# Performance work log

Hardware: AMD Instinct MI355X
Metric: run time of the kernel (lower is better)

## Reference

```python
import jax, jax.numpy as jnp
import numpy as np

D = 128          # feature / hidden dim
K = 3            # SortPooling k (hard-coded in Topkpool)
NUM_CLASS = 10
EPS = 1e-5       # BatchNorm eps


def setup_inputs() -> dict:
    key = jax.random.key(0)
    ks = jax.random.split(key, 24)
    G, NPG = 512, 200
    N = G * NPG
    E = 1638400
    inp = {
        "x": jax.random.normal(ks[0], (N, D), jnp.float32),
        "src": jax.random.randint(ks[1], (E,), 0, N),
        "dst": jax.random.randint(ks[2], (E,), 0, N),
        "num_graphs": G,
        "nodes_per_graph": NPG,
    }
    s = 1.0 / np.sqrt(D)
    for i in (1, 2, 3):
        inp[f"W{i}"] = jax.random.uniform(ks[2 + i], (D, D), jnp.float32, -s, s)
        inp[f"b{i}"] = jnp.zeros((D,), jnp.float32)
        inp[f"g{i}"] = jnp.ones((D,), jnp.float32)   # BN gamma
        inp[f"bt{i}"] = jnp.zeros((D,), jnp.float32)  # BN beta
    sp = 1.0 / np.sqrt(K * D)
    for i in range(4):
        inp[f"P{i}w"] = jax.random.uniform(ks[10 + i], (K * D, NUM_CLASS), jnp.float32, -sp, sp)
        inp[f"P{i}b"] = jnp.zeros((NUM_CLASS,), jnp.float32)
    return inp


def _graph_conv(h, src, dst, W, b, n):
    # DGL GraphConv, norm='both': D_in^{-1/2} A (D_out^{-1/2} h) W + b
    one = jnp.ones((src.shape[0],), h.dtype)
    deg_out = jnp.zeros((n,), h.dtype).at[src].add(one)
    deg_in = jnp.zeros((n,), h.dtype).at[dst].add(one)
    h = h * jax.lax.rsqrt(jnp.maximum(deg_out, 1.0))[:, None]
    agg = jax.ops.segment_sum(h[src], dst, num_segments=n)  # [N, D] scatter-add
    agg = agg * jax.lax.rsqrt(jnp.maximum(deg_in, 1.0))[:, None]
    return agg @ W + b


def _bn_relu(h, g, bt):
    mu = h.mean(axis=0)
    var = jnp.mean((h - mu) ** 2, axis=0)  # biased var, torch BN training mode
    return jax.nn.relu((h - mu) * jax.lax.rsqrt(var + EPS) * g + bt)


def _sort_pool(h, G, npg):
    # DGL SortPooling: sort each node's feature vector ascending, then pick
    # top-K nodes per graph by last (max) channel, concatenate features.
    d = h.shape[-1]
    hs = jnp.sort(h, axis=-1).reshape(G, npg, d)
    idx = jax.lax.top_k(hs[:, :, -1], K)[1]                       # [G, K]
    return jnp.take_along_axis(hs, idx[:, :, None], axis=1).reshape(G, K * d)


def reference(x, W1, b1, g1, bt1, W2, b2, g2, bt2, W3, b3, g3, bt3,
              P0w, P0b, P1w, P1b, P2w, P2b, P3w, P3b,
              src, dst, num_graphs, nodes_per_graph):
    n = x.shape[0]
    reps = [x]
    h = x
    for W, b, g, bt in ((W1, b1, g1, bt1), (W2, b2, g2, bt2), (W3, b3, g3, bt3)):
        h = _bn_relu(_graph_conv(h, src, dst, W, b, n), g, bt)
        reps.append(h)
    score = jnp.zeros((num_graphs, NUM_CLASS), x.dtype)
    for h_i, Pw, Pb in zip(reps, (P0w, P1w, P2w, P3w), (P0b, P1b, P2b, P3b)):
        score = score + _sort_pool(h_i, num_graphs, nodes_per_graph) @ Pw + Pb
    return score
```

## Files before the change

### kernel.cpp

```cpp
#include <hip/hip_runtime.h>
#include <hip/hip_bf16.h>

#define D 128
#define KTOP 3
#define NCLS 10
#define EPS 1e-5f
#define GBM 128
#define BCAP 64


__global__ __launch_bounds__(256) void prologue_kernel(
        const int* __restrict__ src,
        int* __restrict__ deg_out, int E,
        const float* __restrict__ x, float* __restrict__ nodemax, int N,
        float* __restrict__ score, const float* __restrict__ pb0,
        const float* __restrict__ pb1, const float* __restrict__ pb2,
        const float* __restrict__ pb3, int G) {
    int b = blockIdx.x;
    int nbDeg = (E + 255) >> 8;
    if (b < nbDeg) {
        int e = b * 256 + threadIdx.x;
        if (e < E) atomicAdd(&deg_out[src[e]], 1);
        return;
    }
    b -= nbDeg;
    int nbR = N >> 3;
    if (b < nbR) {
        int node = b * 8 + (threadIdx.x >> 5);
        int l = threadIdx.x & 31;
        float4 v = *reinterpret_cast<const float4*>(x + (size_t)node * D + 4 * l);
        float m = fmaxf(fmaxf(v.x, v.y), fmaxf(v.z, v.w));
#pragma unroll
        for (int d = 16; d > 0; d >>= 1) m = fmaxf(m, __shfl_xor(m, d, 64));
        if (l == 0) nodemax[node] = m;
        return;
    }
    for (int i = threadIdx.x; i < G * NCLS; i += 256) {
        int c = i % NCLS;
        score[i] = pb0[c] + pb1[c] + pb2[c] + pb3[c];
    }
}

__global__ void rs_out_kernel(const int* __restrict__ deg_out,
                              float* __restrict__ rs_out, int N) {
    int i = blockIdx.x * blockDim.x + threadIdx.x;
    if (i >= N) return;
    int a = deg_out[i]; if (a < 1) a = 1;
    rs_out[i] = rsqrtf((float)a);
}

__global__ void csr_scatter(const int* __restrict__ src, const int* __restrict__ dst,
                            const float* __restrict__ rs_out,
                            int* __restrict__ cursor, int2* __restrict__ csrw, int E) {
    int e = blockIdx.x * blockDim.x + threadIdx.x;
    if (e >= E) return;
    int d = dst[e], s = src[e];
    int slot = atomicAdd(&cursor[d], 1);
    if (slot >= BCAP) return;
    int2 p; p.x = s; p.y = __float_as_int(rs_out[s]);
    csrw[(size_t)d * BCAP + slot] = p;
}

__global__ void pad_kernel(const int* __restrict__ cursor, int2* __restrict__ csrw, int N) {
    int d = blockIdx.x * blockDim.x + threadIdx.x;
    if (d >= N) return;
    int c = cursor[d]; if (c > BCAP) c = BCAP;
    int end = (c + 7) & ~7;
    int2 z; z.x = 0; z.y = 0;
    for (int i = c; i < end; ++i) csrw[(size_t)d * BCAP + i] = z;
}


__global__ __launch_bounds__(256) void aggregate_head(
        const float* __restrict__ hin, const int* __restrict__ cursor,
        const int2* __restrict__ csrw, float* __restrict__ hout, int nHalf,
        const float* __restrict__ nodemax, const float* __restrict__ Pw,
        float* __restrict__ score, int NPG) {
    __shared__ float ov[256];
    __shared__ float sv[256];
    __shared__ int   si[256];
    __shared__ int   sel[KTOP];
    __shared__ float sbuf[KTOP][D];
    __shared__ float red[4][NCLS];
    int b = blockIdx.x;
    int t = threadIdx.x;
    int nAgg = 2 * nHalf;
    if (b < nAgg) {
        int pass = (b >= nHalf) ? 1 : 0;
        int nb = pass ? b - nHalf : b;
        int node = nb * 16 + (t >> 4);
        int l = t & 15;
        int colOff = (pass << 6) + 4 * l;
        int deg = cursor[node];
        int end = (deg + 7) & ~7;
        const int2* bkt = csrw + (size_t)node * BCAP;
        const float* base = hin + colOff;
        float4 a0 = {0.f, 0.f, 0.f, 0.f}, a1 = a0;
        for (int e = 0; e < end; e += 8) {
            const int4* ce = reinterpret_cast<const int4*>(bkt + e);
            int4 p0 = ce[0], p1 = ce[1], p2 = ce[2], p3 = ce[3];
            float4 v0 = *reinterpret_cast<const float4*>(base + (size_t)p0.x * D);
            float4 v1 = *reinterpret_cast<const float4*>(base + (size_t)p0.z * D);
            float4 v2 = *reinterpret_cast<const float4*>(base + (size_t)p1.x * D);
            float4 v3 = *reinterpret_cast<const float4*>(base + (size_t)p1.z * D);
            float4 v4 = *reinterpret_cast<const float4*>(base + (size_t)p2.x * D);
            float4 v5 = *reinterpret_cast<const float4*>(base + (size_t)p2.z * D);
            float4 v6 = *reinterpret_cast<const float4*>(base + (size_t)p3.x * D);
            float4 v7 = *reinterpret_cast<const float4*>(base + (size_t)p3.z * D);
            float w0 = __int_as_float(p0.y), w1 = __int_as_float(p0.w);
            float w2 = __int_as_float(p1.y), w3 = __int_as_float(p1.w);
            float w4 = __int_as_float(p2.y), w5 = __int_as_float(p2.w);
            float w6 = __int_as_float(p3.y), w7 = __int_as_float(p3.w);
            a0.x += w0*v0.x; a0.y += w0*v0.y; a0.z += w0*v0.z; a0.w += w0*v0.w;
            a1.x += w1*v1.x; a1.y += w1*v1.y; a1.z += w1*v1.z; a1.w += w1*v1.w;
            a0.x += w2*v2.x; a0.y += w2*v2.y; a0.z += w2*v2.z; a0.w += w2*v2.w;
            a1.x += w3*v3.x; a1.y += w3*v3.y; a1.z += w3*v3.z; a1.w += w3*v3.w;
            a0.x += w4*v4.x; a0.y += w4*v4.y; a0.z += w4*v4.z; a0.w += w4*v4.w;
            a1.x += w5*v5.x; a1.y += w5*v5.y; a1.z += w5*v5.z; a1.w += w5*v5.w;
            a0.x += w6*v6.x; a0.y += w6*v6.y; a0.z += w6*v6.z; a0.w += w6*v6.w;
            a1.x += w7*v7.x; a1.y += w7*v7.y; a1.z += w7*v7.z; a1.w += w7*v7.w;
        }
        float ri = rsqrtf((float)(deg < 1 ? 1 : deg));
        float4 r;
        r.x = (a0.x + a1.x) * ri;
        r.y = (a0.y + a1.y) * ri;
        r.z = (a0.z + a1.z) * ri;
        r.w = (a0.w + a1.w) * ri;
        *reinterpret_cast<float4*>(hout + (size_t)node * D + colOff) = r;
        return;
    }

    int gr = b - nAgg;
    ov[t] = (t < NPG) ? nodemax[(size_t)gr * NPG + t] : -3.4e38f;
    __syncthreads();
    for (int ks = 0; ks < KTOP; ++ks) {
        sv[t] = ov[t]; si[t] = t;
        __syncthreads();
        for (int s = 128; s > 0; s >>= 1) {
            if (t < s) {
                float a = sv[t], c = sv[t + s];
                int ia = si[t], ib = si[t + s];
                if (c > a || (c == a && ib < ia)) { sv[t] = c; si[t] = ib; }
            }
            __syncthreads();
        }
        if (t == 0) { sel[ks] = si[0]; ov[si[0]] = -3.4e38f; }
        __syncthreads();
    }
    int u = t >> 7, tl = t & 127;
    sbuf[u][tl] = hin[((size_t)gr * NPG + sel[u]) * D + tl];
    if (t < 128) sbuf[2][t] = hin[((size_t)gr * NPG + sel[2]) * D + t];
    __syncthreads();
    for (int size = 2; size <= D; size <<= 1) {
        for (int stride = size >> 1; stride > 0; stride >>= 1) {
            int ixj = tl ^ stride;
            if (ixj > tl) {
                float a = sbuf[u][tl], c = sbuf[u][ixj];
                bool up = ((tl & size) == 0);
                if ((a > c) == up) { sbuf[u][tl] = c; sbuf[u][ixj] = a; }
            }
            if (t < 128) {
                int ix2 = t ^ stride;
                if (ix2 > t) {
                    float a = sbuf[2][t], c = sbuf[2][ix2];
                    bool up = ((t & size) == 0);
                    if ((a > c) == up) { sbuf[2][t] = c; sbuf[2][ix2] = a; }
                }
            }
            __syncthreads();
        }
    }
    float part[NCLS];
    float v0 = sbuf[u][tl];
    const float* pw0 = Pw + (size_t)(u * D + tl) * NCLS;
#pragma unroll
    for (int c = 0; c < NCLS; ++c) part[c] = v0 * pw0[c];
    if (t < 128) {
        float v2 = sbuf[2][t];
        const float* pw2 = Pw + (size_t)(2 * D + t) * NCLS;
#pragma unroll
        for (int c = 0; c < NCLS; ++c) part[c] += v2 * pw2[c];
    }
    int lane = t & 63, wid = t >> 6;
#pragma unroll
    for (int c = 0; c < NCLS; ++c) {
        float xx = part[c];
#pragma unroll
        for (int o = 32; o > 0; o >>= 1) xx += __shfl_down(xx, o, 64);
        if (lane == 0) red[wid][c] = xx;
    }
    __syncthreads();
    if (t < NCLS)
        atomicAdd(&score[gr * NCLS + t],
                  red[0][t] + red[1][t] + red[2][t] + red[3][t]);
}


__device__ __forceinline__ void gemm_chunk(const float* __restrict__ ain, size_t rowBase,
        int kc, int c0, const float (*Wl)[D], float (&acc)[4][8]) {
#pragma unroll 2
    for (int k4 = 0; k4 < 16; ++k4) {
        const float* ap = ain + rowBase * D + kc + 4 * k4;
        float4 a0 = *reinterpret_cast<const float4*>(ap);
        float4 a1 = *reinterpret_cast<const float4*>(ap + D);
        float4 a2 = *reinterpret_cast<const float4*>(ap + 2 * D);
        float4 a3 = *reinterpret_cast<const float4*>(ap + 3 * D);
#pragma unroll
        for (int j = 0; j < 4; ++j) {
            int kk = 4 * k4 + j;
            float4 w0 = *reinterpret_cast<const float4*>(&Wl[kk][c0]);
            float4 w1 = *reinterpret_cast<const float4*>(&Wl[kk][c0 + 4]);
            float av[4];
            av[0] = (j==0)?a0.x:(j==1)?a0.y:(j==2)?a0.z:a0.w;
            av[1] = (j==0)?a1.x:(j==1)?a1.y:(j==2)?a1.z:a1.w;
            av[2] = (j==0)?a2.x:(j==1)?a2.y:(j==2)?a2.z:a2.w;
            av[3] = (j==0)?a3.x:(j==1)?a3.y:(j==2)?a3.z:a3.w;
            float wv[8] = {w0.x, w0.y, w0.z, w0.w, w1.x, w1.y, w1.z, w1.w};
#pragma unroll
            for (int i = 0; i < 4; ++i)
#pragma unroll
                for (int jj = 0; jj < 8; ++jj) acc[i][jj] += av[i] * wv[jj];
        }
    }
}

__global__ __launch_bounds__(512) void gemm_bn(const float* __restrict__ ain,
        const float* __restrict__ W, const float* __restrict__ bias,
        float* __restrict__ hout, float* __restrict__ bnsums, int N) {
    __shared__ __align__(16) float Wl[64][D];
    int t = threadIdx.x;
    int cg = t & 15;
    int rs = t >> 4;
    int c0 = cg * 8;
    size_t rowBase = (size_t)blockIdx.x * GBM + 4 * rs;

    float acc[4][8];
#pragma unroll
    for (int i = 0; i < 4; ++i)
#pragma unroll
        for (int j = 0; j < 8; ++j) acc[i][j] = 0.f;

    const float4* Wv = reinterpret_cast<const float4*>(W);
    float4* Wd = reinterpret_cast<float4*>(&Wl[0][0]);
    float4 wpre[4];
#pragma unroll
    for (int i = 0; i < 4; ++i) wpre[i] = Wv[t + 512 * i];
#pragma unroll
    for (int i = 0; i < 4; ++i) Wd[t + 512 * i] = wpre[i];
#pragma unroll
    for (int i = 0; i < 4; ++i) wpre[i] = Wv[2048 + t + 512 * i];
    __syncthreads();
    gemm_chunk(ain, rowBase, 0, c0, Wl, acc);
    __syncthreads();
#pragma unroll
    for (int i = 0; i < 4; ++i) Wd[t + 512 * i] = wpre[i];
    __syncthreads();
    gemm_chunk(ain, rowBase, 64, c0, Wl, acc);

    float4 b0 = *reinterpret_cast<const float4*>(&bias[c0]);
    float4 b1 = *reinterpret_cast<const float4*>(&bias[c0 + 4]);
    float bv[8] = {b0.x, b0.y, b0.z, b0.w, b1.x, b1.y, b1.z, b1.w};
    float cs[8], cq[8];
#pragma unroll
    for (int j = 0; j < 8; ++j) { cs[j] = 0.f; cq[j] = 0.f; }
#pragma unroll
    for (int i = 0; i < 4; ++i) {
#pragma unroll
        for (int j = 0; j < 8; ++j) {
            float v = acc[i][j] + bv[j];
            acc[i][j] = v;
            cs[j] += v;
            cq[j] += v * v;
        }
    }
#pragma unroll
    for (int i = 0; i < 4; ++i) {
        size_t row = rowBase + i;
        float4 o0, o1;
        o0.x = acc[i][0]; o0.y = acc[i][1]; o0.z = acc[i][2]; o0.w = acc[i][3];
        o1.x = acc[i][4]; o1.y = acc[i][5]; o1.z = acc[i][6]; o1.w = acc[i][7];
        *reinterpret_cast<float4*>(&hout[row * D + c0])     = o0;
        *reinterpret_cast<float4*>(&hout[row * D + c0 + 4]) = o1;
    }
#pragma unroll
    for (int j = 0; j < 8; ++j) {
        cs[j] += __shfl_xor(cs[j], 16, 64); cq[j] += __shfl_xor(cq[j], 16, 64);
        cs[j] += __shfl_xor(cs[j], 32, 64); cq[j] += __shfl_xor(cq[j], 32, 64);
    }
    __syncthreads();
    float* red = &Wl[0][0];
    int wid = t >> 6, lane = t & 63;
    if (lane < 16) {
#pragma unroll
        for (int j = 0; j < 8; ++j) {
            red[wid * 256 + lane * 16 + j]     = cs[j];
            red[wid * 256 + lane * 16 + 8 + j] = cq[j];
        }
    }
    __syncthreads();
    if (t < 256) {
        float s = 0.f;
#pragma unroll
        for (int w = 0; w < 8; ++w) s += red[w * 256 + t];
        int cgi = t >> 4, r = t & 15;
        int ch = cgi * 8 + (r & 7);
        atomicAdd(&bnsums[(r < 8 ? 0 : D) + ch], s);
    }
}


__global__ __launch_bounds__(256) void bn_apply_relu_max(float* __restrict__ h,
        const float* __restrict__ bnsums, const float* __restrict__ g,
        const float* __restrict__ bt, float* __restrict__ nodemax, int N, float invN) {
    __shared__ float sc[D], sh[D];
    int t = threadIdx.x;
    if (t < D) {
        float mu  = bnsums[t] * invN;
        float var = bnsums[D + t] * invN - mu * mu;
        float inv = rsqrtf(var + EPS);
        float s = g[t] * inv;
        sc[t] = s;
        sh[t] = bt[t] - mu * s;
    }
    __syncthreads();
    int node = (blockIdx.x * 256 + t) >> 5;
    int l = t & 31;
    if (node >= N) return;
    float4 v = *reinterpret_cast<const float4*>(h + (size_t)node * D + 4 * l);
    float4 a = *reinterpret_cast<const float4*>(&sc[4 * l]);
    float4 b = *reinterpret_cast<const float4*>(&sh[4 * l]);
    v.x = fmaxf(fmaf(v.x, a.x, b.x), 0.f);
    v.y = fmaxf(fmaf(v.y, a.y, b.y), 0.f);
    v.z = fmaxf(fmaf(v.z, a.z, b.z), 0.f);
    v.w = fmaxf(fmaf(v.w, a.w, b.w), 0.f);
    *reinterpret_cast<float4*>(h + (size_t)node * D + 4 * l) = v;
    float m = fmaxf(fmaxf(v.x, v.y), fmaxf(v.z, v.w));
#pragma unroll
    for (int d = 16; d > 0; d >>= 1) m = fmaxf(m, __shfl_xor(m, d, 64));
    if (l == 0) nodemax[node] = m;
}


extern "C" void kernel_launch(void* const* d_in, const int* in_sizes, int n_in,
                              void* d_out, int out_size, void* d_ws, size_t ws_size,
                              hipStream_t stream) {
    const float* x   = (const float*)d_in[0];
    const int*   src = (const int*)d_in[1];
    const int*   dst = (const int*)d_in[2];
    const float* W[3]  = {(const float*)d_in[5],  (const float*)d_in[9],  (const float*)d_in[13]};
    const float* bb[3] = {(const float*)d_in[6],  (const float*)d_in[10], (const float*)d_in[14]};
    const float* gg[3] = {(const float*)d_in[7],  (const float*)d_in[11], (const float*)d_in[15]};
    const float* bt[3] = {(const float*)d_in[8],  (const float*)d_in[12], (const float*)d_in[16]};
    const float* Pw[4] = {(const float*)d_in[17], (const float*)d_in[19], (const float*)d_in[21], (const float*)d_in[23]};
    const float* Pb[4] = {(const float*)d_in[18], (const float*)d_in[20], (const float*)d_in[22], (const float*)d_in[24]};

    int N = in_sizes[0] / D;
    int E = in_sizes[1];
    int G = out_size / NCLS;
    int NPG = N / G;
    float* score = (float*)d_out;

    size_t NF = (size_t)N * D;
    float* fws     = (float*)d_ws;
    float* H       = fws;
    float* T       = H + NF;
    float* rs_out  = T + NF;
    float* nodemax = rs_out + N;
    float* bnsums  = nodemax + N;
    int* deg_out = (int*)(bnsums + 6 * D);
    int* cursor  = deg_out + N;
    int2* csrw   = (int2*)(cursor + N);

    int nbDeg = (E + 255) >> 8;
    int nbR = N >> 3;
    float invN = 1.0f / (float)N;

    hipMemsetAsync(deg_out, 0, sizeof(int) * (size_t)2 * N, stream);
    hipMemsetAsync(bnsums, 0, sizeof(float) * 6 * D, stream);

    prologue_kernel<<<nbDeg + nbR + 1, 256, 0, stream>>>(
        src, deg_out, E, x, nodemax, N,
        score, Pb[0], Pb[1], Pb[2], Pb[3], G);
    rs_out_kernel<<<(N + 255) / 256, 256, 0, stream>>>(deg_out, rs_out, N);
    csr_scatter<<<(E + 255) / 256, 256, 0, stream>>>(src, dst, rs_out, cursor, csrw, E);
    pad_kernel<<<(N + 255) / 256, 256, 0, stream>>>(cursor, csrw, N);

    int nHalf = N / 16;
    const float* hin = x;
    for (int l = 0; l < 3; ++l) {
        float* bns = bnsums + l * 2 * D;
        aggregate_head<<<2 * nHalf + G, 256, 0, stream>>>(
            hin, cursor, csrw, T, nHalf, nodemax, Pw[l], score, NPG);
        gemm_bn<<<N / GBM, 512, 0, stream>>>(T, W[l], bb[l], H, bns, N);
        bn_apply_relu_max<<<N / 8, 256, 0, stream>>>(H, bns, gg[l], bt[l], nodemax, N, invN);
        hin = H;
    }
    aggregate_head<<<G, 256, 0, stream>>>(
        H, cursor, csrw, T, 0, nodemax, Pw[3], score, NPG);
}
```

Before: 830.7 us.

## Fuse CSR build into prologue, defer weight fill, widen aggregation to full rows

The dst-bucketed CSR scatter now runs inside the prologue kernel alongside the out-degree count, and only source indices are stored. A new wfill_pad kernel fills the rsqrt(deg_out) weights and zero-pads each bucket, which removes the rs_out array and two separate launches. Aggregation now uses 32 lanes per node covering all 128 columns instead of two half-column passes, so each bucket's index list is read once rather than twice. The capped loop bound also avoids overrunning a bucket when the degree exceeds BCAP.

```diff
diff --git a/kernel.cpp b/kernel.cpp
--- a/kernel.cpp
+++ b/kernel.cpp
@@ -10,8 +10,9 @@
 
 
 __global__ __launch_bounds__(256) void prologue_kernel(
-        const int* __restrict__ src,
-        int* __restrict__ deg_out, int E,
+        const int* __restrict__ src, const int* __restrict__ dst,
+        int* __restrict__ deg_out, int* __restrict__ cursor,
+        int2* __restrict__ csrw, int E,
         const float* __restrict__ x, float* __restrict__ nodemax, int N,
         float* __restrict__ score, const float* __restrict__ pb0,
         const float* __restrict__ pb1, const float* __restrict__ pb2,
@@ -24,6 +25,17 @@
         return;
     }
     b -= nbDeg;
+    if (b < nbDeg) {
+        int e = b * 256 + threadIdx.x;
+        if (e < E) {
+            int d = dst[e];
+            int slot = atomicAdd(&cursor[d], 1);
+            if (slot < BCAP)
+                reinterpret_cast<int*>(csrw)[((size_t)d * BCAP + slot) * 2] = src[e];
+        }
+        return;
+    }
+    b -= nbDeg;
     int nbR = N >> 3;
     if (b < nbR) {
         int node = b * 8 + (threadIdx.x >> 5);
@@ -41,39 +53,29 @@
     }
 }
 
-__global__ void rs_out_kernel(const int* __restrict__ deg_out,
-                              float* __restrict__ rs_out, int N) {
-    int i = blockIdx.x * blockDim.x + threadIdx.x;
-    if (i >= N) return;
-    int a = deg_out[i]; if (a < 1) a = 1;
-    rs_out[i] = rsqrtf((float)a);
-}
-
-__global__ void csr_scatter(const int* __restrict__ src, const int* __restrict__ dst,
-                            const float* __restrict__ rs_out,
-                            int* __restrict__ cursor, int2* __restrict__ csrw, int E) {
-    int e = blockIdx.x * blockDim.x + threadIdx.x;
-    if (e >= E) return;
-    int d = dst[e], s = src[e];
-    int slot = atomicAdd(&cursor[d], 1);
-    if (slot >= BCAP) return;
-    int2 p; p.x = s; p.y = __float_as_int(rs_out[s]);
-    csrw[(size_t)d * BCAP + slot] = p;
-}
-
-__global__ void pad_kernel(const int* __restrict__ cursor, int2* __restrict__ csrw, int N) {
-    int d = blockIdx.x * blockDim.x + threadIdx.x;
-    if (d >= N) return;
-    int c = cursor[d]; if (c > BCAP) c = BCAP;
-    int end = (c + 7) & ~7;
-    int2 z; z.x = 0; z.y = 0;
-    for (int i = c; i < end; ++i) csrw[(size_t)d * BCAP + i] = z;
+
+__global__ __launch_bounds__(256) void wfill_pad(const int* __restrict__ cursor,
+        const int* __restrict__ deg_out, int2* __restrict__ csrw, int N) {
+    int node = blockIdx.x * 4 + (threadIdx.x >> 6);
+    int slot = threadIdx.x & 63;
+    if (node >= N) return;
+    int c = cursor[node]; if (c > BCAP) c = BCAP;
+    int cpad = (c + 7) & ~7;
+    int2* ent = csrw + (size_t)node * BCAP + slot;
+    if (slot < c) {
+        int s = ent->x;
+        int dg = deg_out[s]; if (dg < 1) dg = 1;
+        ent->y = __float_as_int(rsqrtf((float)dg));
+    } else if (slot < cpad) {
+        int2 z; z.x = 0; z.y = 0;
+        *ent = z;
+    }
 }
 
 
 __global__ __launch_bounds__(256) void aggregate_head(
         const float* __restrict__ hin, const int* __restrict__ cursor,
-        const int2* __restrict__ csrw, float* __restrict__ hout, int nHalf,
+        const int2* __restrict__ csrw, float* __restrict__ hout, int nAgg,
         const float* __restrict__ nodemax, const float* __restrict__ Pw,
         float* __restrict__ score, int NPG) {
     __shared__ float ov[256];
@@ -84,17 +86,13 @@
     __shared__ float red[4][NCLS];
     int b = blockIdx.x;
     int t = threadIdx.x;
-    int nAgg = 2 * nHalf;
     if (b < nAgg) {
-        int pass = (b >= nHalf) ? 1 : 0;
-        int nb = pass ? b - nHalf : b;
-        int node = nb * 16 + (t >> 4);
-        int l = t & 15;
-        int colOff = (pass << 6) + 4 * l;
+        int node = b * 8 + (t >> 5);
+        int l = t & 31;
         int deg = cursor[node];
-        int end = (deg + 7) & ~7;
+        int end = (deg + 7) & ~7; if (end > BCAP) end = BCAP;
         const int2* bkt = csrw + (size_t)node * BCAP;
-        const float* base = hin + colOff;
+        const float* base = hin + 4 * l;
         float4 a0 = {0.f, 0.f, 0.f, 0.f}, a1 = a0;
         for (int e = 0; e < end; e += 8) {
             const int4* ce = reinterpret_cast<const int4*>(bkt + e);
@@ -126,7 +124,7 @@
         r.y = (a0.y + a1.y) * ri;
         r.z = (a0.z + a1.z) * ri;
         r.w = (a0.w + a1.w) * ri;
-        *reinterpret_cast<float4*>(hout + (size_t)node * D + colOff) = r;
+        *reinterpret_cast<float4*>(hout + (size_t)node * D + 4 * l) = r;
         return;
     }
 
@@ -364,8 +362,7 @@
     float* fws     = (float*)d_ws;
     float* H       = fws;
     float* T       = H + NF;
-    float* rs_out  = T + NF;
-    float* nodemax = rs_out + N;
+    float* nodemax = T + NF;
     float* bnsums  = nodemax + N;
     int* deg_out = (int*)(bnsums + 6 * D);
     int* cursor  = deg_out + N;
@@ -378,19 +375,17 @@
     hipMemsetAsync(deg_out, 0, sizeof(int) * (size_t)2 * N, stream);
     hipMemsetAsync(bnsums, 0, sizeof(float) * 6 * D, stream);
 
-    prologue_kernel<<<nbDeg + nbR + 1, 256, 0, stream>>>(
-        src, deg_out, E, x, nodemax, N,
+    prologue_kernel<<<2 * nbDeg + nbR + 1, 256, 0, stream>>>(
+        src, dst, deg_out, cursor, csrw, E, x, nodemax, N,
         score, Pb[0], Pb[1], Pb[2], Pb[3], G);
-    rs_out_kernel<<<(N + 255) / 256, 256, 0, stream>>>(deg_out, rs_out, N);
-    csr_scatter<<<(E + 255) / 256, 256, 0, stream>>>(src, dst, rs_out, cursor, csrw, E);
-    pad_kernel<<<(N + 255) / 256, 256, 0, stream>>>(cursor, csrw, N);
-
-    int nHalf = N / 16;
+    wfill_pad<<<(N + 3) / 4, 256, 0, stream>>>(cursor, deg_out, csrw, N);
+
+    int nAgg = N / 8;
     const float* hin = x;
     for (int l = 0; l < 3; ++l) {
         float* bns = bnsums + l * 2 * D;
-        aggregate_head<<<2 * nHalf + G, 256, 0, stream>>>(
-            hin, cursor, csrw, T, nHalf, nodemax, Pw[l], score, NPG);
+        aggregate_head<<<nAgg + G, 256, 0, stream>>>(
+            hin, cursor, csrw, T, nAgg, nodemax, Pw[l], score, NPG);
         gemm_bn<<<N / GBM, 512, 0, stream>>>(T, W[l], bb[l], H, bns, N);
         bn_apply_relu_max<<<N / 8, 256, 0, stream>>>(H, bns, gg[l], bt[l], nodemax, N, invN);
         hin = H;
```

Measured after the change: 881.6 us. +6.1%, slower.

## Fuse BN+ReLU into neighbor gather, drop rs_out kernel, widen aggregation

Applied to the files above, without the earlier changes.

Stops writing the normalized activations back in the BN kernel, which now only computes node maxima. Instead the BN scale/shift and ReLU are applied on the fly to each gathered neighbor row in the next aggregation, and to the selected rows in the sort-pool head. This saves a full read+write pass over the N×D activation tensor per layer, at the cost of extra FMAs on every gathered edge (E×D instead of N×D). Also folds the rs_out computation into csr_scatter, and switches the aggregation from two 64-column passes to a single pass with 32 lanes per node.

```diff
diff --git a/kernel.cpp b/kernel.cpp
--- a/kernel.cpp
+++ b/kernel.cpp
@@ -41,23 +41,16 @@
     }
 }
 
-__global__ void rs_out_kernel(const int* __restrict__ deg_out,
-                              float* __restrict__ rs_out, int N) {
-    int i = blockIdx.x * blockDim.x + threadIdx.x;
-    if (i >= N) return;
-    int a = deg_out[i]; if (a < 1) a = 1;
-    rs_out[i] = rsqrtf((float)a);
-}
-
 __global__ void csr_scatter(const int* __restrict__ src, const int* __restrict__ dst,
-                            const float* __restrict__ rs_out,
+                            const int* __restrict__ deg_out,
                             int* __restrict__ cursor, int2* __restrict__ csrw, int E) {
     int e = blockIdx.x * blockDim.x + threadIdx.x;
     if (e >= E) return;
     int d = dst[e], s = src[e];
     int slot = atomicAdd(&cursor[d], 1);
     if (slot >= BCAP) return;
-    int2 p; p.x = s; p.y = __float_as_int(rs_out[s]);
+    int dg = deg_out[s]; if (dg < 1) dg = 1;
+    int2 p; p.x = s; p.y = __float_as_int(rsqrtf((float)dg));
     csrw[(size_t)d * BCAP + slot] = p;
 }
 
@@ -70,31 +63,56 @@
     for (int i = c; i < end; ++i) csrw[(size_t)d * BCAP + i] = z;
 }
 
+__device__ __forceinline__ float4 bnrelu4(float4 v, float4 sc, float4 sh) {
+    float4 r;
+    r.x = fmaxf(fmaf(v.x, sc.x, sh.x), 0.f);
+    r.y = fmaxf(fmaf(v.y, sc.y, sh.y), 0.f);
+    r.z = fmaxf(fmaf(v.z, sc.z, sh.z), 0.f);
+    r.w = fmaxf(fmaf(v.w, sc.w, sh.w), 0.f);
+    return r;
+}
+
 
 __global__ __launch_bounds__(256) void aggregate_head(
         const float* __restrict__ hin, const int* __restrict__ cursor,
-        const int2* __restrict__ csrw, float* __restrict__ hout, int nHalf,
+        const int2* __restrict__ csrw, float* __restrict__ hout, int nAgg,
         const float* __restrict__ nodemax, const float* __restrict__ Pw,
-        float* __restrict__ score, int NPG) {
+        float* __restrict__ score, int NPG,
+        const float* __restrict__ bns, const float* __restrict__ g,
+        const float* __restrict__ bt, float invN) {
     __shared__ float ov[256];
     __shared__ float sv[256];
     __shared__ int   si[256];
     __shared__ int   sel[KTOP];
     __shared__ float sbuf[KTOP][D];
     __shared__ float red[4][NCLS];
+    __shared__ float scs[D], shs[D];
     int b = blockIdx.x;
     int t = threadIdx.x;
-    int nAgg = 2 * nHalf;
+    bool useBN = (bns != nullptr);
+    if (useBN) {
+        if (t < D) {
+            float mu  = bns[t] * invN;
+            float var = bns[D + t] * invN - mu * mu;
+            float inv = rsqrtf(var + EPS);
+            float s = g[t] * inv;
+            scs[t] = s;
+            shs[t] = bt[t] - mu * s;
+        }
+        __syncthreads();
+    }
     if (b < nAgg) {
-        int pass = (b >= nHalf) ? 1 : 0;
-        int nb = pass ? b - nHalf : b;
-        int node = nb * 16 + (t >> 4);
-        int l = t & 15;
-        int colOff = (pass << 6) + 4 * l;
+        int node = b * 8 + (t >> 5);
+        int l = t & 31;
         int deg = cursor[node];
-        int end = (deg + 7) & ~7;
+        int end = (deg + 7) & ~7; if (end > BCAP) end = BCAP;
         const int2* bkt = csrw + (size_t)node * BCAP;
-        const float* base = hin + colOff;
+        const float* base = hin + 4 * l;
+        float4 sc4, sh4;
+        if (useBN) {
+            sc4 = *reinterpret_cast<const float4*>(&scs[4 * l]);
+            sh4 = *reinterpret_cast<const float4*>(&shs[4 * l]);
+        }
         float4 a0 = {0.f, 0.f, 0.f, 0.f}, a1 = a0;
         for (int e = 0; e < end; e += 8) {
             const int4* ce = reinterpret_cast<const int4*>(bkt + e);
@@ -107,6 +125,12 @@
             float4 v5 = *reinterpret_cast<const float4*>(base + (size_t)p2.z * D);
             float4 v6 = *reinterpret_cast<const float4*>(base + (size_t)p3.x * D);
             float4 v7 = *reinterpret_cast<const float4*>(base + (size_t)p3.z * D);
+            if (useBN) {
+                v0 = bnrelu4(v0, sc4, sh4); v1 = bnrelu4(v1, sc4, sh4);
+                v2 = bnrelu4(v2, sc4, sh4); v3 = bnrelu4(v3, sc4, sh4);
+                v4 = bnrelu4(v4, sc4, sh4); v5 = bnrelu4(v5, sc4, sh4);
+                v6 = bnrelu4(v6, sc4, sh4); v7 = bnrelu4(v7, sc4, sh4);
+            }
             float w0 = __int_as_float(p0.y), w1 = __int_as_float(p0.w);
             float w2 = __int_as_float(p1.y), w3 = __int_as_float(p1.w);
             float w4 = __int_as_float(p2.y), w5 = __int_as_float(p2.w);
@@ -126,7 +150,7 @@
         r.y = (a0.y + a1.y) * ri;
         r.z = (a0.z + a1.z) * ri;
         r.w = (a0.w + a1.w) * ri;
-        *reinterpret_cast<float4*>(hout + (size_t)node * D + colOff) = r;
+        *reinterpret_cast<float4*>(hout + (size_t)node * D + 4 * l) = r;
         return;
     }
 
@@ -148,8 +172,14 @@
         __syncthreads();
     }
     int u = t >> 7, tl = t & 127;
-    sbuf[u][tl] = hin[((size_t)gr * NPG + sel[u]) * D + tl];
-    if (t < 128) sbuf[2][t] = hin[((size_t)gr * NPG + sel[2]) * D + t];
+    {
+        float v = hin[((size_t)gr * NPG + sel[u]) * D + tl];
+        sbuf[u][tl] = useBN ? fmaxf(fmaf(v, scs[tl], shs[tl]), 0.f) : v;
+        if (t < 128) {
+            float v2 = hin[((size_t)gr * NPG + sel[2]) * D + t];
+            sbuf[2][t] = useBN ? fmaxf(fmaf(v2, scs[t], shs[t]), 0.f) : v2;
+        }
+    }
     __syncthreads();
     for (int size = 2; size <= D; size <<= 1) {
         for (int stride = size >> 1; stride > 0; stride >>= 1) {
@@ -309,7 +339,7 @@
 }
 
 
-__global__ __launch_bounds__(256) void bn_apply_relu_max(float* __restrict__ h,
+__global__ __launch_bounds__(256) void bn_nodemax(const float* __restrict__ h,
         const float* __restrict__ bnsums, const float* __restrict__ g,
         const float* __restrict__ bt, float* __restrict__ nodemax, int N, float invN) {
     __shared__ float sc[D], sh[D];
@@ -333,7 +363,6 @@
     v.y = fmaxf(fmaf(v.y, a.y, b.y), 0.f);
     v.z = fmaxf(fmaf(v.z, a.z, b.z), 0.f);
     v.w = fmaxf(fmaf(v.w, a.w, b.w), 0.f);
-    *reinterpret_cast<float4*>(h + (size_t)node * D + 4 * l) = v;
     float m = fmaxf(fmaxf(v.x, v.y), fmaxf(v.z, v.w));
 #pragma unroll
     for (int d = 16; d > 0; d >>= 1) m = fmaxf(m, __shfl_xor(m, d, 64));
@@ -364,8 +393,7 @@
     float* fws     = (float*)d_ws;
     float* H       = fws;
     float* T       = H + NF;
-    float* rs_out  = T + NF;
-    float* nodemax = rs_out + N;
+    float* nodemax = T + NF;
     float* bnsums  = nodemax + N;
     int* deg_out = (int*)(bnsums + 6 * D);
     int* cursor  = deg_out + N;
@@ -381,20 +409,25 @@
     prologue_kernel<<<nbDeg + nbR + 1, 256, 0, stream>>>(
         src, deg_out, E, x, nodemax, N,
         score, Pb[0], Pb[1], Pb[2], Pb[3], G);
-    rs_out_kernel<<<(N + 255) / 256, 256, 0, stream>>>(deg_out, rs_out, N);
-    csr_scatter<<<(E + 255) / 256, 256, 0, stream>>>(src, dst, rs_out, cursor, csrw, E);
+    csr_scatter<<<(E + 255) / 256, 256, 0, stream>>>(src, dst, deg_out, cursor, csrw, E);
     pad_kernel<<<(N + 255) / 256, 256, 0, stream>>>(cursor, csrw, N);
 
-    int nHalf = N / 16;
+    int nAgg = N / 8;
     const float* hin = x;
+    const float* curBns = nullptr;
+    const float* curG = nullptr;
+    const float* curBt = nullptr;
     for (int l = 0; l < 3; ++l) {
         float* bns = bnsums + l * 2 * D;
-        aggregate_head<<<2 * nHalf + G, 256, 0, stream>>>(
-            hin, cursor, csrw, T, nHalf, nodemax, Pw[l], score, NPG);
+        aggregate_head<<<nAgg + G, 256, 0, stream>>>(
+            hin, cursor, csrw, T, nAgg, nodemax, Pw[l], score, NPG,
+            curBns, curG, curBt, invN);
         gemm_bn<<<N / GBM, 512, 0, stream>>>(T, W[l], bb[l], H, bns, N);
-        bn_apply_relu_max<<<N / 8, 256, 0, stream>>>(H, bns, gg[l], bt[l], nodemax, N, invN);
+        bn_nodemax<<<N / 8, 256, 0, stream>>>(H, bns, gg[l], bt[l], nodemax, N, invN);
         hin = H;
+        curBns = bns; curG = gg[l]; curBt = bt[l];
     }
     aggregate_head<<<G, 256, 0, stream>>>(
-        H, cursor, csrw, T, 0, nodemax, Pw[3], score, NPG);
-}
+        H, cursor, csrw, T, 0, nodemax, Pw[3], score, NPG,
+        curBns, curG, curBt, invN);
+}
```

Result: no change. 833.7 us (+0.4%).
